# Performance work log

Measured on AMD Instinct MI355X. Metric: run time of the kernel, lower is better.

## Reference

```python
import jax, jax.numpy as jnp
import numpy as np

NEG = -1e30  # finite stand-in for -inf (keeps grads nan-free)
BLANK = 0


def _ctc_nll(log_probs, targets, input_lengths, target_lengths):
    """Per-sample CTC negative log-likelihood.
    log_probs: (B,T,V) log-softmax outputs; targets: (B,S) int; lengths: (B,)."""
    B, T, V = log_probs.shape
    S = targets.shape[1]
    L = 2 * S + 1
    # extended label sequence: blank, y1, blank, y2, ..., blank -> (B, L)
    ext = jnp.full((B, L), BLANK, dtype=targets.dtype).at[:, 1::2].set(targets)
    # skip transition (l-2 -> l) allowed iff ext[l] != blank and ext[l] != ext[l-2]
    prev2 = jnp.pad(ext[:, :-2], ((0, 0), (2, 0)), constant_values=-1)
    skip = (ext != BLANK) & (ext != prev2)  # (B, L)

    def emit(lp_t):  # lp_t: (B,V) -> (B,L)
        return jnp.take_along_axis(lp_t, ext, axis=1)

    alpha0 = jnp.where(jnp.arange(L)[None, :] < 2, emit(log_probs[:, 0]), NEG)

    def step(alpha, lp_t):
        p1 = jnp.pad(alpha[:, :-1], ((0, 0), (1, 0)), constant_values=NEG)
        p2 = jnp.pad(alpha[:, :-2], ((0, 0), (2, 0)), constant_values=NEG)
        p2 = jnp.where(skip, p2, NEG)
        m = jnp.maximum(alpha, jnp.maximum(p1, p2))
        lse = m + jnp.log(jnp.exp(alpha - m) + jnp.exp(p1 - m) + jnp.exp(p2 - m))
        new = lse + emit(lp_t)
        return new, new

    # scan over time; collect alphas so we can read them at each sample's T_b-1
    _, alphas_rest = jax.lax.scan(step, alpha0, jnp.swapaxes(log_probs, 0, 1)[1:])
    alphas = jnp.concatenate([alpha0[None], alphas_rest], axis=0)  # (T,B,L)
    alphas = jnp.swapaxes(alphas, 0, 1)  # (B,T,L)
    alpha_T = jnp.take_along_axis(
        alphas, (input_lengths - 1)[:, None, None], axis=1)[:, 0]  # (B,L)

    end1 = jnp.take_along_axis(alpha_T, (2 * target_lengths)[:, None], axis=1)[:, 0]
    end2 = jnp.take_along_axis(alpha_T, (2 * target_lengths - 1)[:, None], axis=1)[:, 0]
    m = jnp.maximum(end1, end2)
    ll = m + jnp.log(jnp.exp(end1 - m) + jnp.exp(end2 - m))
    return -ll  # (B,)


def setup_inputs() -> dict:
    key = jax.random.key(0)
    k1, k2, k3, k4 = jax.random.split(key, 4)
    B, T, V, S = 32, 2000, 1024, 256
    log_probs = jax.nn.log_softmax(
        jax.random.normal(k1, (B, T, V), dtype=jnp.float32), axis=-1)
    targets = jax.random.randint(k2, (B, S), 1, V)  # exclude blank=0
    input_lengths = jax.random.randint(k3, (B,), 1500, T + 1)
    target_lengths = jax.random.randint(k4, (B,), 128, S + 1)
    return {"log_probs": log_probs, "targets": targets,
            "input_lengths": input_lengths, "target_lengths": target_lengths}


def reference(log_probs, targets, input_lengths, target_lengths):
    nll = _ctc_nll(log_probs, targets, input_lengths, target_lengths)
    # zero_infinity=True: drop infeasible samples
    nll = jnp.where(nll > 0.5 * (-NEG), 0.0, nll)
    # reduction='mean': divide each loss by its target length, then batch-mean
    return jnp.mean(nll / target_lengths.astype(nll.dtype))
```

## Files before the change

kernel.cpp:

```cpp
#include <hip/hip_runtime.h>
#include <stdint.h>


#define LN2F 0.69314718055994530942f
#define NR 16

#define ASYNC_CP16(g, l)                                                     \
  __builtin_amdgcn_global_load_lds(                                          \
      (__attribute__((address_space(1))) void*)(g),                          \
      (__attribute__((address_space(3))) void*)(l), 16, 0, 0)
#define ASYNC_CP4(g, l)                                                      \
  __builtin_amdgcn_global_load_lds(                                          \
      (__attribute__((address_space(1))) void*)(g),                          \
      (__attribute__((address_space(3))) void*)(l), 4, 0, 0)

__device__ __forceinline__ float shr1f(float x) {
  return __int_as_float(
      __builtin_amdgcn_update_dpp(0, __float_as_int(x), 0x138, 0xF, 0xF, true));
}
__device__ __forceinline__ int shr1i(int x) {
  return __builtin_amdgcn_update_dpp(0, x, 0x138, 0xF, 0xF, true);
}

__global__ __launch_bounds__(256) void k_gather_exp(
    const float* __restrict__ lp, const int* __restrict__ tgt,
    const int* __restrict__ ilen, float* __restrict__ El,
    float* __restrict__ Eb, int T, int V, int S) {
  const int b = blockIdx.y;
  const int t = blockIdx.x;
  if (t >= ilen[b]) return;
  const int tid = threadIdx.x;
  const int lab = tgt[b * S + tid];
  const float* row = lp + ((size_t)b * T + t) * V;
  El[((size_t)b * T + t) * S + tid] = __expf(row[lab]);
  if (tid == 0) Eb[(size_t)b * T + t] = __expf(row[0]);
}

__global__ __launch_bounds__(64) void k_ctc_alpha(
    const float* __restrict__ El, const float* __restrict__ Eb,
    const int* __restrict__ tgt, const int* __restrict__ ilen,
    const int* __restrict__ tlen, float* __restrict__ nll_out, int T, int S) {
  const int b = blockIdx.x;
  const int lane = threadIdx.x;
  const bool l0 = (lane == 0);
  __shared__ __align__(16) float elbuf[2][NR][256];
  __shared__ __align__(16) float ebbuf[2][NR];

  const int Tb = ilen[b];
  const int U = tlen[b];

  const int4 tg = *(const int4*)(tgt + (size_t)b * S + 4 * lane);
  const int tprev = __shfl_up(tg.w, 1);
  const float sk0 = (l0 || tg.x != tprev) ? 1.0f : 0.0f;
  const float sk1 = (tg.y != tg.x) ? 1.0f : 0.0f;
  const float sk2 = (tg.z != tg.y) ? 1.0f : 0.0f;
  const float sk3 = (tg.w != tg.z) ? 1.0f : 0.0f;

  const float* Elb = El + (size_t)b * T * 256;
  const float* Ebb = Eb + (size_t)b * T;
  const int lo4 = 4 * lane;

  float a0 = 0, aL0 = 0, aL1 = 0, aL2 = 0, aL3 = 0;
  float aB0 = 0, aB1 = 0, aB2 = 0, aB3 = 0;
  int o = 0;
  float s = 1.0f;

  auto issue_chunk = [&](int c, int buf) {
    const int base = c * NR;
#pragma unroll
    for (int r = 0; r < NR; ++r) {
      const int row = min(base + r, Tb - 1);
      ASYNC_CP16(Elb + ((size_t)row << 8) + lo4, &elbuf[buf][r][0]);
    }
    const int erow = min(base + (int)lane, Tb - 1);
    if (lane < NR) ASYNC_CP4(Ebb + erow, &ebbuf[buf][0]);
  };

  auto stepf = [&](float4 el, float eb) {
    const float pL = shr1f(aL3) * s;
    float pB = shr1f(aB3) * s;
    pB = l0 ? a0 : pB;
    const float nB0 = (aB0 + aL0) * eb;
    const float nB1 = (aB1 + aL1) * eb;
    const float nB2 = (aB2 + aL2) * eb;
    const float nB3 = (aB3 + aL3) * eb;
    const float nL0 = (aL0 + fmaf(sk0, pL, pB)) * el.x;
    const float nL1 = (aL1 + fmaf(sk1, aL0, aB0)) * el.y;
    const float nL2 = (aL2 + fmaf(sk2, aL1, aB1)) * el.z;
    const float nL3 = (aL3 + fmaf(sk3, aL2, aB2)) * el.w;
    a0 *= eb;
    aL0 = nL0; aL1 = nL1; aL2 = nL2; aL3 = nL3;
    aB0 = nB0; aB1 = nB1; aB2 = nB2; aB3 = nB3;
  };
  auto renorm = [&]() {
    float m = fmaxf(fmaxf(fmaxf(aL0, aL1), fmaxf(aL2, aL3)),
                    fmaxf(fmaxf(aB0, aB1), fmaxf(aB2, aB3)));
    m = fmaxf(m, a0);
    const bool nz = (m > 0.0f);
    const int mk = nz ? (((__float_as_int(m) >> 23) & 0xff) - 126) : 0;
    const int ocand = o + mk;
    const int oleft = shr1i(ocand);
    o = (nz || l0) ? ocand : oleft;
    const float sc = nz ? __int_as_float((127 - mk) << 23) : 1.0f;
    aL0 *= sc; aL1 *= sc; aL2 *= sc; aL3 *= sc;
    aB0 *= sc; aB1 *= sc; aB2 *= sc; aB3 *= sc;
    a0 *= sc;
    int d = shr1i(o) - o;
    d = max(-126, min(126, d));
    s = __int_as_float((d + 127) << 23);
  };

  issue_chunk(0, 0);
  const int nchunks = (Tb + NR - 1) / NR;

  for (int c = 0; c < nchunks; ++c) {
    const int buf = c & 1;
    if (c + 1 < nchunks) {
      issue_chunk(c + 1, buf ^ 1);
      asm volatile("s_waitcnt vmcnt(17)" ::: "memory");
    } else {
      asm volatile("s_waitcnt vmcnt(0)" ::: "memory");
    }
    const int jend = min(NR, Tb - c * NR);
    if (jend == NR) {
#pragma unroll
      for (int j = 0; j < NR; ++j) {
        const float4 el = *(const float4*)&elbuf[buf][j][lo4];
        const float eb = ebbuf[buf][j];
        if (c == 0 && j == 0) {
          a0 = l0 ? eb : 0.0f;
          aL0 = l0 ? el.x : 0.0f;
        } else {
          stepf(el, eb);
        }
        if ((j & 3) == 3) renorm();
      }
    } else {
      for (int j = 0; j < jend; ++j) {
        const float4 el = *(const float4*)&elbuf[buf][j][lo4];
        const float eb = ebbuf[buf][j];
        if (c == 0 && j == 0) {
          a0 = l0 ? eb : 0.0f;
          aL0 = l0 ? el.x : 0.0f;
        } else {
          stepf(el, eb);
        }
        if ((j & 3) == 3) renorm();
      }
    }
  }

  if (lane == ((U - 1) >> 2)) {
    const int j = (U - 1) & 3;
    float sv;
    if (j == 0)      sv = aL0 + aB0;
    else if (j == 1) sv = aL1 + aB1;
    else if (j == 2) sv = aL2 + aB2;
    else             sv = aL3 + aB3;
    float nll = -LN2F * (__log2f(sv) + (float)o);
    if (!(nll < 5e29f)) nll = 0.0f;
    nll_out[b] = nll / (float)U;
  }
}

__global__ __launch_bounds__(64) void k_reduce(const float* __restrict__ nll,
                                               float* __restrict__ out,
                                               int B) {
  float v = 0.0f;
  for (int i = threadIdx.x; i < B; i += 64) v += nll[i];
  for (int off = 32; off > 0; off >>= 1) v += __shfl_down(v, off);
  if (threadIdx.x == 0) out[0] = v / (float)B;
}

extern "C" void kernel_launch(void* const* d_in, const int* in_sizes, int n_in,
                              void* d_out, int out_size, void* d_ws,
                              size_t ws_size, hipStream_t stream) {
  const float* lp = (const float*)d_in[0];
  const int* tgt = (const int*)d_in[1];
  const int* ilen = (const int*)d_in[2];
  const int* tlen = (const int*)d_in[3];

  const int B = in_sizes[2];
  const int S = in_sizes[1] / B;
  const int V = 1024;
  const int T = (int)((size_t)in_sizes[0] / ((size_t)B * V));

  float* El = (float*)d_ws;
  float* Eb = El + (size_t)B * T * S;
  float* nw = Eb + (size_t)B * T;

  dim3 g1(T, B);
  k_gather_exp<<<g1, 256, 0, stream>>>(lp, tgt, ilen, El, Eb, T, V, S);
  k_ctc_alpha<<<B, 64, 0, stream>>>(El, Eb, tgt, ilen, tlen, nw, T, S);
  k_reduce<<<1, 64, 0, stream>>>(nw, (float*)d_out, B);
}
```

Before: 536.1 us.

## Replace LDS async double-buffer with register double-buffered prefetch in CTC alpha kernel

The alpha recursion kernel stops staging emission probabilities through LDS with global_load_lds and now loads each 16-step chunk straight into register arrays, alternating between two register buffers. Blank emissions are loaded one per lane and broadcast with readlane instead of being read from LDS. A sched_barrier keeps the prefetch loads issued ahead of the serial compute, and launch bounds are set to one block per SM so more registers are available. This removes the LDS round-trip and its wait counts from the latency-bound serial loop, at the cost of high register pressure (about 128 extra VGPRs) and reliance on the compiler inserting correct vmcnt waits.

```diff
diff --git a/kernel.cpp b/kernel.cpp
--- a/kernel.cpp
+++ b/kernel.cpp
@@ -5,21 +5,15 @@
 #define LN2F 0.69314718055994530942f
 #define NR 16
 
-#define ASYNC_CP16(g, l)                                                     \
-  __builtin_amdgcn_global_load_lds(                                          \
-      (__attribute__((address_space(1))) void*)(g),                          \
-      (__attribute__((address_space(3))) void*)(l), 16, 0, 0)
-#define ASYNC_CP4(g, l)                                                      \
-  __builtin_amdgcn_global_load_lds(                                          \
-      (__attribute__((address_space(1))) void*)(g),                          \
-      (__attribute__((address_space(3))) void*)(l), 4, 0, 0)
-
 __device__ __forceinline__ float shr1f(float x) {
   return __int_as_float(
       __builtin_amdgcn_update_dpp(0, __float_as_int(x), 0x138, 0xF, 0xF, true));
 }
 __device__ __forceinline__ int shr1i(int x) {
   return __builtin_amdgcn_update_dpp(0, x, 0x138, 0xF, 0xF, true);
+}
+__device__ __forceinline__ float rlanef(float v, int l) {
+  return __int_as_float(__builtin_amdgcn_readlane(__float_as_int(v), l));
 }
 
 __global__ __launch_bounds__(256) void k_gather_exp(
@@ -36,15 +30,13 @@
   if (tid == 0) Eb[(size_t)b * T + t] = __expf(row[0]);
 }
 
-__global__ __launch_bounds__(64) void k_ctc_alpha(
+__global__ __launch_bounds__(64, 1) void k_ctc_alpha(
     const float* __restrict__ El, const float* __restrict__ Eb,
     const int* __restrict__ tgt, const int* __restrict__ ilen,
     const int* __restrict__ tlen, float* __restrict__ nll_out, int T, int S) {
   const int b = blockIdx.x;
   const int lane = threadIdx.x;
   const bool l0 = (lane == 0);
-  __shared__ __align__(16) float elbuf[2][NR][256];
-  __shared__ __align__(16) float ebbuf[2][NR];
 
   const int Tb = ilen[b];
   const int U = tlen[b];
@@ -64,17 +56,6 @@
   float aB0 = 0, aB1 = 0, aB2 = 0, aB3 = 0;
   int o = 0;
   float s = 1.0f;
-
-  auto issue_chunk = [&](int c, int buf) {
-    const int base = c * NR;
-#pragma unroll
-    for (int r = 0; r < NR; ++r) {
-      const int row = min(base + r, Tb - 1);
-      ASYNC_CP16(Elb + ((size_t)row << 8) + lo4, &elbuf[buf][r][0]);
-    }
-    const int erow = min(base + (int)lane, Tb - 1);
-    if (lane < NR) ASYNC_CP4(Ebb + erow, &ebbuf[buf][0]);
-  };
 
   auto stepf = [&](float4 el, float eb) {
     const float pL = shr1f(aL3) * s;
@@ -110,44 +91,61 @@
     s = __int_as_float((d + 127) << 23);
   };
 
-  issue_chunk(0, 0);
-  const int nchunks = (Tb + NR - 1) / NR;
+  float4 elA[NR], elB[NR];
+  float ebA, ebB;
 
-  for (int c = 0; c < nchunks; ++c) {
-    const int buf = c & 1;
-    if (c + 1 < nchunks) {
-      issue_chunk(c + 1, buf ^ 1);
-      asm volatile("s_waitcnt vmcnt(17)" ::: "memory");
-    } else {
-      asm volatile("s_waitcnt vmcnt(0)" ::: "memory");
+  auto load_chunk = [&](int c, float4* el, float& ebv) {
+    const int base = c * NR;
+    const int erow = min(base + lane, Tb - 1);
+    ebv = Ebb[erow];
+#pragma unroll
+    for (int r = 0; r < NR; ++r) {
+      const int row = min(base + r, Tb - 1);
+      el[r] = *(const float4*)(Elb + ((size_t)row << 8) + lo4);
     }
-    const int jend = min(NR, Tb - c * NR);
-    if (jend == NR) {
+  };
+
+  auto consume_full = [&](bool first, const float4* el, float ebv) {
 #pragma unroll
-      for (int j = 0; j < NR; ++j) {
-        const float4 el = *(const float4*)&elbuf[buf][j][lo4];
-        const float eb = ebbuf[buf][j];
-        if (c == 0 && j == 0) {
-          a0 = l0 ? eb : 0.0f;
-          aL0 = l0 ? el.x : 0.0f;
-        } else {
-          stepf(el, eb);
-        }
-        if ((j & 3) == 3) renorm();
+    for (int j = 0; j < NR; ++j) {
+      const float eb = rlanef(ebv, j);
+      if (j == 0 && first) {
+        a0 = l0 ? eb : 0.0f;
+        aL0 = l0 ? el[0].x : 0.0f;
+      } else {
+        stepf(el[j], eb);
       }
-    } else {
-      for (int j = 0; j < jend; ++j) {
-        const float4 el = *(const float4*)&elbuf[buf][j][lo4];
-        const float eb = ebbuf[buf][j];
-        if (c == 0 && j == 0) {
-          a0 = l0 ? eb : 0.0f;
-          aL0 = l0 ? el.x : 0.0f;
-        } else {
-          stepf(el, eb);
-        }
+      if ((j & 3) == 3) renorm();
+    }
+  };
+  auto consume_tail = [&](const float4* el, float ebv, int jend) {
+#pragma unroll
+    for (int j = 0; j < NR; ++j) {
+      if (j < jend) {
+        stepf(el[j], rlanef(ebv, j));
         if ((j & 3) == 3) renorm();
       }
     }
+  };
+
+  const int nchunks = (Tb + NR - 1) / NR;
+  load_chunk(0, elA, ebA);
+  int c = 0;
+  for (; c + 1 < nchunks; ++c) {
+    if ((c & 1) == 0) {
+      load_chunk(c + 1, elB, ebB);
+      __builtin_amdgcn_sched_barrier(0);
+      consume_full(c == 0, elA, ebA);
+    } else {
+      load_chunk(c + 1, elA, ebA);
+      __builtin_amdgcn_sched_barrier(0);
+      consume_full(false, elB, ebB);
+    }
+  }
+  {
+    const int jend = Tb - c * NR;
+    if ((c & 1) == 0) consume_tail(elA, ebA, jend);
+    else              consume_tail(elB, ebB, jend);
   }
 
   if (lane == ((U - 1) >> 2)) {
```

Measured after the change: 527.2 us. Within noise of the previous version (-1.7%).
